# Kernel tuning notes

Hardware: AMD Instinct MI355X
Metric: run time of the kernel (lower is better)

The kernel has to match this reference:

```python
import jax, jax.numpy as jnp
import numpy as np

B, H, S, D = 4, 8, 2048, 64

def setup_inputs() -> dict:
    key = jax.random.key(0)
    k1, k2 = jax.random.split(key)
    q = jax.random.normal(k1, (B, H, S, D), dtype=jnp.float32)
    kv = jax.random.normal(k2, (B, H, S, D), dtype=jnp.float32)
    mask = jnp.zeros((1, 1, S, S), dtype=jnp.float32)
    return {"q": q, "kv": kv, "mask": mask}

def reference(q, kv, mask):
    # score = q @ kv^T / sqrt(d_k) + mask ; softmax over last dim ; @ kv
    d_k = jnp.asarray(kv.shape[-1], dtype=q.dtype)
    score = jnp.einsum('bhqd,bhkd->bhqk', q, kv) / jnp.sqrt(d_k)
    score = score + mask
    attn = jax.nn.softmax(score, axis=-1)
    out = jnp.einsum('bhqk,bhkd->bhqd', attn, kv)
    return out
```

## Files before the change

kernel.cpp:

```cpp
#include <hip/hip_runtime.h>
#include <hip/hip_bf16.h>
#include <stdint.h>


typedef __bf16 bf16;
typedef __attribute__((ext_vector_type(8))) __bf16 bf16x8;
typedef __attribute__((ext_vector_type(4))) __bf16 bf16x4;
typedef __attribute__((ext_vector_type(4))) float floatx4;
typedef __attribute__((ext_vector_type(16))) float floatx16;
typedef __attribute__((ext_vector_type(4))) int int4v;
typedef __attribute__((ext_vector_type(2))) unsigned int uint2v;

#define SLEN 2048
#define DH   64
#define BR   64
#define BC   64
#define NKT  (SLEN / BC)
#define NQT  (SLEN / BR)
#define BH_N 32
#define LOG2E 1.44269504088896341f

#define IMGE_G 4096

#define AS1 __attribute__((address_space(1)))
#define AS3 __attribute__((address_space(3)))

static __device__ inline float fexp2(float x) {
    return __builtin_amdgcn_exp2f(x);
}

static_assert(BH_N == NQT, "prep kernel folds bh and qt onto one grid axis");

__global__ __launch_bounds__(256) void kv_prep(
    const float* __restrict__ kv, const float* __restrict__ mask,
    bf16* __restrict__ kvK, bf16* __restrict__ kvT, int* __restrict__ flags)
{
    __shared__ bf16 Tl[64 * 72];
    __shared__ int wany[4];
    const int kt = blockIdx.x, z = blockIdx.y;
    const int t = threadIdx.x;

    float acc = 0.f;
#pragma unroll
    for (int i = 0; i < 4; ++i) {
        int f = i * 256 + t;
        int row = f >> 4, c4 = (f & 15) * 4;
        const float4 v = *(const float4*)(mask + (size_t)(z * BR + row) * SLEN + kt * BC + c4);
        acc = fmaxf(acc, fmaxf(fmaxf(fabsf(v.x), fabsf(v.y)), fmaxf(fabsf(v.z), fabsf(v.w))));
    }
    unsigned long long any = __ballot(acc != 0.f);
    if ((t & 63) == 0) wany[t >> 6] = (any != 0ull) ? 1 : 0;

    const float* src = kv + ((size_t)z * SLEN + kt * BC) * DH;
#pragma unroll
    for (int i = 0; i < 4; ++i) {
        int f = i * 256 + t;
        int key = f >> 4, d4 = (f & 15) * 4;
        float4 v = *(const float4*)(src + (size_t)key * DH + d4);
        bf16x4 b; b[0] = (bf16)v.x; b[1] = (bf16)v.y; b[2] = (bf16)v.z; b[3] = (bf16)v.w;
        *(bf16x4*)&Tl[key * 72 + d4] = b;
    }
    __syncthreads();
    if (t == 0) flags[z * NKT + kt] = wany[0] | wany[1] | wany[2] | wany[3];

    bf16* outK = kvK + ((size_t)z * NKT + kt) * IMGE_G;
#pragma unroll
    for (int i = 0; i < 2; ++i) {
        int G = i * 256 + t;
        int u = G >> 8, ss = (G >> 6) & 3, ln = G & 63;
        int key = u * 32 + (ln & 31), d0 = 16 * ss + 8 * (ln >> 5);
        bf16x8 w = *(const bf16x8*)&Tl[key * 72 + d0];
        *(bf16x8*)(outK + (size_t)G * 8) = w;
    }
    bf16* outV = kvT + ((size_t)z * NKT + kt) * IMGE_G;
#pragma unroll
    for (int i = 0; i < 2; ++i) {
        int G = i * 256 + t;
        int dt = G >> 8, u = (G >> 7) & 1, ff = (G >> 6) & 1, ln = G & 63;
        int d = dt * 32 + (ln & 31), kb = u * 32 + 16 * ff + 8 * (ln >> 5);
        bf16x8 w;
#pragma unroll
        for (int j = 0; j < 8; ++j)
            w[j] = Tl[(kb + j) * 72 + d];
        *(bf16x8*)(outV + (size_t)G * 8) = w;
    }
}

__global__ __launch_bounds__(512, 2) void attn_fwd19(
    const float* __restrict__ q, const float* __restrict__ mask,
    const int* __restrict__ flags,
    const bf16* __restrict__ kvK, const bf16* __restrict__ kvT,
    float* __restrict__ out)
{
    __shared__ __align__(16) float Obuf[4 * 2 * 4 * 64 * 4];
    __shared__ float Lbuf[4 * 64];

    const int bh = blockIdx.x;
    const int qt = blockIdx.y;
    const int q0 = qt * 128;
    const int t = threadIdx.x;
    const int w = t >> 6, lane = t & 63;
    const int qg = w & 3, kh = w >> 2;
    const int r5 = lane & 31, h = lane >> 5;

    const float qscale = 0.125f * LOG2E;
    bf16x8 qf[4];
    {
        const float* qrow = q + ((size_t)bh * SLEN + q0 + qg * 32 + r5) * DH;
#pragma unroll
        for (int s = 0; s < 4; ++s) {
            float4 f0 = *(const float4*)(qrow + 16 * s + 8 * h);
            float4 f1 = *(const float4*)(qrow + 16 * s + 8 * h + 4);
            bf16x8 a;
            a[0] = (bf16)(f0.x * qscale); a[1] = (bf16)(f0.y * qscale);
            a[2] = (bf16)(f0.z * qscale); a[3] = (bf16)(f0.w * qscale);
            a[4] = (bf16)(f1.x * qscale); a[5] = (bf16)(f1.y * qscale);
            a[6] = (bf16)(f1.z * qscale); a[7] = (bf16)(f1.w * qscale);
            qf[s] = a;
        }
    }

    const int fqt = qt * 2 + (qg >> 1);
    unsigned fmask;
    {
        int ld = (lane < 32) ? flags[fqt * NKT + lane] : 0;
        fmask = (unsigned)__ballot(ld != 0);
    }

    floatx16 o[2];
#pragma unroll
    for (int dt = 0; dt < 2; ++dt)
#pragma unroll
        for (int i = 0; i < 16; ++i) o[dt][i] = 0.f;
    float l_run = 0.f;

    const char* Kb = (const char*)(kvK + (size_t)bh * NKT * IMGE_G) + lane * 16;
    const char* Vb = (const char*)(kvT + (size_t)bh * NKT * IMGE_G) + lane * 16;

    for (int e = 0; e < 16; ++e) {
        const int kt = kh * 16 + e;
        const char* Kt = Kb + (size_t)kt * 8192;
        const char* Vt = Vb + (size_t)kt * 8192;
        const bool dm = (fmask >> kt) & 1u;

#pragma unroll
        for (int u = 0; u < 2; ++u) {
            floatx16 s;
#pragma unroll
            for (int i = 0; i < 16; ++i) s[i] = 0.f;
            {
                const char* Ku = Kt + u * 4096;
                bf16x8 kf0 = *(const bf16x8*)(Ku);
                bf16x8 kf1 = *(const bf16x8*)(Ku + 1024);
                bf16x8 kf2 = *(const bf16x8*)(Ku + 2048);
                bf16x8 kf3 = *(const bf16x8*)(Ku + 3072);
                s = __builtin_amdgcn_mfma_f32_32x32x16_bf16(kf0, qf[0], s, 0, 0, 0);
                s = __builtin_amdgcn_mfma_f32_32x32x16_bf16(kf1, qf[1], s, 0, 0, 0);
                s = __builtin_amdgcn_mfma_f32_32x32x16_bf16(kf2, qf[2], s, 0, 0, 0);
                s = __builtin_amdgcn_mfma_f32_32x32x16_bf16(kf3, qf[3], s, 0, 0, 0);
            }

            if (dm) {
                const float* mrow = mask + (size_t)(q0 + qg * 32 + r5) * SLEN
                                    + kt * 64 + u * 32 + 4 * h;
#pragma unroll
                for (int g4 = 0; g4 < 4; ++g4) {
                    float4 mv = *(const float4*)(mrow + 8 * g4);
                    s[4 * g4 + 0] += mv.x * LOG2E;
                    s[4 * g4 + 1] += mv.y * LOG2E;
                    s[4 * g4 + 2] += mv.z * LOG2E;
                    s[4 * g4 + 3] += mv.w * LOG2E;
                }
            }

            const char* Vu = Vt + u * 2048;
            bf16x8 v00 = *(const bf16x8*)(Vu);
            bf16x8 v01 = *(const bf16x8*)(Vu + 1024);
            bf16x8 v10 = *(const bf16x8*)(Vu + 4096);
            bf16x8 v11 = *(const bf16x8*)(Vu + 4096 + 1024);

#pragma unroll
            for (int i = 0; i < 16; ++i) s[i] = fexp2(s[i]);
            l_run += ((s[0] + s[1]) + (s[2] + s[3]))
                   + ((s[4] + s[5]) + (s[6] + s[7]))
                   + ((s[8] + s[9]) + (s[10] + s[11]))
                   + ((s[12] + s[13]) + (s[14] + s[15]));

            bf16x4 lA = { (bf16)s[0],  (bf16)s[1],  (bf16)s[2],  (bf16)s[3]  };
            bf16x4 hA = { (bf16)s[4],  (bf16)s[5],  (bf16)s[6],  (bf16)s[7]  };
            bf16x4 lB = { (bf16)s[8],  (bf16)s[9],  (bf16)s[10], (bf16)s[11] };
            bf16x4 hB = { (bf16)s[12], (bf16)s[13], (bf16)s[14], (bf16)s[15] };
            uint2v xA = __builtin_bit_cast(uint2v, lA);
            uint2v yA = __builtin_bit_cast(uint2v, hA);
            uint2v xB = __builtin_bit_cast(uint2v, lB);
            uint2v yB = __builtin_bit_cast(uint2v, hB);
            uint2v sA0 = __builtin_amdgcn_permlane32_swap(xA[0], yA[0], false, false);
            uint2v sA1 = __builtin_amdgcn_permlane32_swap(xA[1], yA[1], false, false);
            uint2v sB0 = __builtin_amdgcn_permlane32_swap(xB[0], yB[0], false, false);
            uint2v sB1 = __builtin_amdgcn_permlane32_swap(xB[1], yB[1], false, false);
            int4v pAi = { (int)sA0[0], (int)sA1[0], (int)sA0[1], (int)sA1[1] };
            int4v pBi = { (int)sB0[0], (int)sB1[0], (int)sB0[1], (int)sB1[1] };
            bf16x8 pfA = __builtin_bit_cast(bf16x8, pAi);
            bf16x8 pfB = __builtin_bit_cast(bf16x8, pBi);

            o[0] = __builtin_amdgcn_mfma_f32_32x32x16_bf16(v00, pfA, o[0], 0, 0, 0);
            o[0] = __builtin_amdgcn_mfma_f32_32x32x16_bf16(v01, pfB, o[0], 0, 0, 0);
            o[1] = __builtin_amdgcn_mfma_f32_32x32x16_bf16(v10, pfA, o[1], 0, 0, 0);
            o[1] = __builtin_amdgcn_mfma_f32_32x32x16_bf16(v11, pfB, o[1], 0, 0, 0);
        }
    }

    __syncthreads();
    if (kh == 1) {
#pragma unroll
        for (int dt = 0; dt < 2; ++dt)
#pragma unroll
            for (int k = 0; k < 4; ++k) {
                float4 v;
                v.x = o[dt][4 * k + 0]; v.y = o[dt][4 * k + 1];
                v.z = o[dt][4 * k + 2]; v.w = o[dt][4 * k + 3];
                *(float4*)(Obuf + ((size_t)((qg * 2 + dt) * 4 + k) * 64 + lane) * 4) = v;
            }
        Lbuf[qg * 64 + lane] = l_run;
    }
    __syncthreads();
    if (kh == 0) {
        float lsum = l_run + Lbuf[qg * 64 + lane];
        float l = lsum + __shfl_xor(lsum, 32);
        float inv = 1.f / l;
        float* ob = out + ((size_t)bh * SLEN + q0 + qg * 32 + r5) * DH + 4 * h;
#pragma unroll
        for (int dt = 0; dt < 2; ++dt)
#pragma unroll
            for (int k = 0; k < 4; ++k) {
                float4 p = *(const float4*)(Obuf + ((size_t)((qg * 2 + dt) * 4 + k) * 64 + lane) * 4);
                float4 v;
                v.x = (o[dt][4 * k + 0] + p.x) * inv;
                v.y = (o[dt][4 * k + 1] + p.y) * inv;
                v.z = (o[dt][4 * k + 2] + p.z) * inv;
                v.w = (o[dt][4 * k + 3] + p.w) * inv;
                *(float4*)(ob + dt * 32 + 8 * k) = v;
            }
    }
}

#define LDT 72
__global__ __launch_bounds__(256) void attn_mask_flags(
    const float* __restrict__ mask, int* __restrict__ flags)
{
    const int kt = blockIdx.x, qt = blockIdx.y;
    const int t = threadIdx.x;
    float acc = 0.f;
#pragma unroll
    for (int i = 0; i < 4; ++i) {
        int f = i * 256 + t;
        int row = f >> 4, c4 = (f & 15) * 4;
        const float4 v = *(const float4*)(mask + (size_t)(qt * BR + row) * SLEN + kt * BC + c4);
        acc = fmaxf(acc, fmaxf(fmaxf(fabsf(v.x), fabsf(v.y)), fmaxf(fabsf(v.z), fabsf(v.w))));
    }
    unsigned long long any = __ballot(acc != 0.f);
    __shared__ int wany[4];
    if ((t & 63) == 0) wany[t >> 6] = (any != 0ull) ? 1 : 0;
    __syncthreads();
    if (t == 0) flags[qt * NKT + kt] = wany[0] | wany[1] | wany[2] | wany[3];
}

__global__ __launch_bounds__(256) void attn_fwd(
    const float* __restrict__ q, const float* __restrict__ kv,
    const float* __restrict__ mask, const int* __restrict__ flags,
    float* __restrict__ out)
{
    __shared__ __align__(16) bf16 Kl[BC * LDT];
    __shared__ __align__(16) bf16 Vt[DH * LDT];
    __shared__ __align__(16) bf16 Pl[BR * LDT];

    const int qt = blockIdx.x;
    const int bh = blockIdx.y;
    const int q0 = qt * BR;
    const int t = threadIdx.x;
    const int wave = t >> 6, lane = t & 63;
    const int ln16 = lane & 15, quad = lane >> 4;

    const float qscale = 0.125f * LOG2E;
    bf16x8 aq[2];
    {
        const float* qrow = q + ((size_t)bh * SLEN + q0 + wave * 16 + ln16) * DH;
#pragma unroll
        for (int kc = 0; kc < 2; ++kc) {
            float4 f0 = *(const float4*)(qrow + kc * 32 + quad * 8);
            float4 f1 = *(const float4*)(qrow + kc * 32 + quad * 8 + 4);
            bf16x8 a;
            a[0] = (bf16)(f0.x * qscale); a[1] = (bf16)(f0.y * qscale);
            a[2] = (bf16)(f0.z * qscale); a[3] = (bf16)(f0.w * qscale);
            a[4] = (bf16)(f1.x * qscale); a[5] = (bf16)(f1.y * qscale);
            a[6] = (bf16)(f1.z * qscale); a[7] = (bf16)(f1.w * qscale);
            aq[kc] = a;
        }
    }

    floatx4 o[4];
#pragma unroll
    for (int dt = 0; dt < 4; ++dt) o[dt] = (floatx4){0.f, 0.f, 0.f, 0.f};
    float m_run[4], l_run[4];
#pragma unroll
    for (int r = 0; r < 4; ++r) { m_run[r] = -3.0e38f; l_run[r] = 0.f; }

    const float* kvb = kv + (size_t)bh * SLEN * DH;

    for (int kt = 0; kt < NKT; ++kt) {
        float4 st[4];
        const float* kvt = kvb + (size_t)kt * BC * DH;
#pragma unroll
        for (int i = 0; i < 4; ++i) {
            int f = i * 256 + t;
            st[i] = *(const float4*)(kvt + (size_t)f * 4);
        }
        __syncthreads();
#pragma unroll
        for (int i = 0; i < 4; ++i) {
            int f = i * 256 + t;
            int key = f >> 4, d4 = (f & 15) * 4;
            bf16 b0 = (bf16)st[i].x, b1 = (bf16)st[i].y, b2 = (bf16)st[i].z, b3 = (bf16)st[i].w;
            *(bf16x4*)&Kl[key * LDT + d4] = (bf16x4){b0, b1, b2, b3};
            Vt[(d4 + 0) * LDT + key] = b0;
            Vt[(d4 + 1) * LDT + key] = b1;
            Vt[(d4 + 2) * LDT + key] = b2;
            Vt[(d4 + 3) * LDT + key] = b3;
        }
        __syncthreads();

        floatx4 s[4];
#pragma unroll
        for (int nt = 0; nt < 4; ++nt) {
            s[nt] = (floatx4){0.f, 0.f, 0.f, 0.f};
#pragma unroll
            for (int kc = 0; kc < 2; ++kc) {
                bf16x8 bk = *(const bf16x8*)&Kl[(ln16 + 16 * nt) * LDT + kc * 32 + quad * 8];
                s[nt] = __builtin_amdgcn_mfma_f32_16x16x32_bf16(aq[kc], bk, s[nt], 0, 0, 0);
            }
        }

        if (!flags || flags[qt * NKT + kt]) {
            const float* mrow = mask + (size_t)(q0 + quad * 4) * SLEN + kt * BC + ln16;
#pragma unroll
            for (int r = 0; r < 4; ++r)
#pragma unroll
                for (int nt = 0; nt < 4; ++nt)
                    s[nt][r] += mrow[(size_t)r * SLEN + nt * 16] * LOG2E;
        }

#pragma unroll
        for (int r = 0; r < 4; ++r) {
            float mx = fmaxf(fmaxf(s[0][r], s[1][r]), fmaxf(s[2][r], s[3][r]));
            mx = fmaxf(mx, __shfl_xor(mx, 1));
            mx = fmaxf(mx, __shfl_xor(mx, 2));
            mx = fmaxf(mx, __shfl_xor(mx, 4));
            mx = fmaxf(mx, __shfl_xor(mx, 8));
            float mnew = fmaxf(m_run[r], mx);
            float alpha = exp2f(m_run[r] - mnew);
            m_run[r] = mnew;
            float rs = 0.f;
#pragma unroll
            for (int nt = 0; nt < 4; ++nt) {
                float p = exp2f(s[nt][r] - mnew);
                s[nt][r] = p;
                rs += p;
            }
            rs += __shfl_xor(rs, 1);
            rs += __shfl_xor(rs, 2);
            rs += __shfl_xor(rs, 4);
            rs += __shfl_xor(rs, 8);
            l_run[r] = l_run[r] * alpha + rs;
#pragma unroll
            for (int dt = 0; dt < 4; ++dt) o[dt][r] *= alpha;
        }

#pragma unroll
        for (int nt = 0; nt < 4; ++nt)
#pragma unroll
            for (int r = 0; r < 4; ++r)
                Pl[(wave * 16 + quad * 4 + r) * LDT + ln16 + 16 * nt] = (bf16)s[nt][r];

#pragma unroll
        for (int kc2 = 0; kc2 < 2; ++kc2) {
            bf16x8 pfr = *(const bf16x8*)&Pl[(wave * 16 + ln16) * LDT + kc2 * 32 + quad * 8];
#pragma unroll
            for (int dt = 0; dt < 4; ++dt) {
                bf16x8 vfr = *(const bf16x8*)&Vt[(ln16 + 16 * dt) * LDT + kc2 * 32 + quad * 8];
                o[dt] = __builtin_amdgcn_mfma_f32_16x16x32_bf16(pfr, vfr, o[dt], 0, 0, 0);
            }
        }
    }

#pragma unroll
    for (int r = 0; r < 4; ++r) {
        float inv = 1.0f / l_run[r];
        int qrow = q0 + wave * 16 + quad * 4 + r;
        float* orow = out + ((size_t)bh * SLEN + qrow) * DH;
#pragma unroll
        for (int dt = 0; dt < 4; ++dt)
            orow[ln16 + 16 * dt] = o[dt][r] * inv;
    }
}

extern "C" void kernel_launch(void* const* d_in, const int* in_sizes, int n_in,
                              void* d_out, int out_size, void* d_ws, size_t ws_size,
                              hipStream_t stream)
{
    const float* q    = (const float*)d_in[0];
    const float* kv   = (const float*)d_in[1];
    const float* mask = (const float*)d_in[2];
    float* out = (float*)d_out;

    const size_t kvKoff = 4096;
    const size_t kvToff = kvKoff + (size_t)BH_N * NKT * IMGE_G * 2;
    const size_t need   = kvToff + (size_t)BH_N * NKT * IMGE_G * 2;

    if (ws_size >= need) {
        int*  flags = (int*)d_ws;
        bf16* kvK   = (bf16*)((char*)d_ws + kvKoff);
        bf16* kvT   = (bf16*)((char*)d_ws + kvToff);
        kv_prep<<<dim3(NKT, BH_N), 256, 0, stream>>>(kv, mask, kvK, kvT, flags);
        attn_fwd19<<<dim3(BH_N, SLEN / 128), 512, 0, stream>>>(q, mask, flags, kvK, kvT, out);
    } else {
        int* flags = nullptr;
        if (ws_size >= (size_t)NQT * NKT * sizeof(int)) {
            flags = (int*)d_ws;
            attn_mask_flags<<<dim3(NKT, NQT), 256, 0, stream>>>(mask, flags);
        }
        attn_fwd<<<dim3(NQT, BH_N), 256, 0, stream>>>(q, kv, mask, flags, out);
    }
}
```

Baseline: 136.4 us.

## Shrink attention blocks to 64 query rows and double-buffer K/V register loads

The attention kernel now uses 256-thread blocks covering 64 query rows instead of 512 threads over 128 rows, doubling the grid size and halving shared memory per block. The key loop is restructured into a software pipeline: K and V fragments for the next sub-tile are loaded into a second register set while the current one is computed. The aim is to hide global-load latency and improve occupancy, at the cost of more registers for the double buffer and each block reusing K/V across fewer query rows.

```diff
diff --git a/kernel.cpp b/kernel.cpp
--- a/kernel.cpp
+++ b/kernel.cpp
@@ -86,21 +86,21 @@
     }
 }
 
-__global__ __launch_bounds__(512, 2) void attn_fwd19(
+__global__ __launch_bounds__(256) void attn_fwd20(
     const float* __restrict__ q, const float* __restrict__ mask,
     const int* __restrict__ flags,
     const bf16* __restrict__ kvK, const bf16* __restrict__ kvT,
     float* __restrict__ out)
 {
-    __shared__ __align__(16) float Obuf[4 * 2 * 4 * 64 * 4];
-    __shared__ float Lbuf[4 * 64];
+    __shared__ __align__(16) float Obuf[2 * 2 * 4 * 64 * 4];
+    __shared__ float Lbuf[2 * 64];
 
     const int bh = blockIdx.x;
     const int qt = blockIdx.y;
-    const int q0 = qt * 128;
+    const int q0 = qt * 64;
     const int t = threadIdx.x;
     const int w = t >> 6, lane = t & 63;
-    const int qg = w & 3, kh = w >> 2;
+    const int qg = w & 1, kh = w >> 1;
     const int r5 = lane & 31, h = lane >> 5;
 
     const float qscale = 0.125f * LOG2E;
@@ -120,10 +120,9 @@
         }
     }
 
-    const int fqt = qt * 2 + (qg >> 1);
     unsigned fmask;
     {
-        int ld = (lane < 32) ? flags[fqt * NKT + lane] : 0;
+        int ld = (lane < 32) ? flags[qt * NKT + lane] : 0;
         fmask = (unsigned)__ballot(ld != 0);
     }
 
@@ -137,78 +136,86 @@
     const char* Kb = (const char*)(kvK + (size_t)bh * NKT * IMGE_G) + lane * 16;
     const char* Vb = (const char*)(kvT + (size_t)bh * NKT * IMGE_G) + lane * 16;
 
-    for (int e = 0; e < 16; ++e) {
-        const int kt = kh * 16 + e;
-        const char* Kt = Kb + (size_t)kt * 8192;
-        const char* Vt = Vb + (size_t)kt * 8192;
-        const bool dm = (fmask >> kt) & 1u;
-
-#pragma unroll
-        for (int u = 0; u < 2; ++u) {
-            floatx16 s;
-#pragma unroll
-            for (int i = 0; i < 16; ++i) s[i] = 0.f;
-            {
-                const char* Ku = Kt + u * 4096;
-                bf16x8 kf0 = *(const bf16x8*)(Ku);
-                bf16x8 kf1 = *(const bf16x8*)(Ku + 1024);
-                bf16x8 kf2 = *(const bf16x8*)(Ku + 2048);
-                bf16x8 kf3 = *(const bf16x8*)(Ku + 3072);
-                s = __builtin_amdgcn_mfma_f32_32x32x16_bf16(kf0, qf[0], s, 0, 0, 0);
-                s = __builtin_amdgcn_mfma_f32_32x32x16_bf16(kf1, qf[1], s, 0, 0, 0);
-                s = __builtin_amdgcn_mfma_f32_32x32x16_bf16(kf2, qf[2], s, 0, 0, 0);
-                s = __builtin_amdgcn_mfma_f32_32x32x16_bf16(kf3, qf[3], s, 0, 0, 0);
-            }
-
-            if (dm) {
-                const float* mrow = mask + (size_t)(q0 + qg * 32 + r5) * SLEN
-                                    + kt * 64 + u * 32 + 4 * h;
-#pragma unroll
-                for (int g4 = 0; g4 < 4; ++g4) {
-                    float4 mv = *(const float4*)(mrow + 8 * g4);
-                    s[4 * g4 + 0] += mv.x * LOG2E;
-                    s[4 * g4 + 1] += mv.y * LOG2E;
-                    s[4 * g4 + 2] += mv.z * LOG2E;
-                    s[4 * g4 + 3] += mv.w * LOG2E;
-                }
-            }
-
-            const char* Vu = Vt + u * 2048;
-            bf16x8 v00 = *(const bf16x8*)(Vu);
-            bf16x8 v01 = *(const bf16x8*)(Vu + 1024);
-            bf16x8 v10 = *(const bf16x8*)(Vu + 4096);
-            bf16x8 v11 = *(const bf16x8*)(Vu + 4096 + 1024);
-
-#pragma unroll
-            for (int i = 0; i < 16; ++i) s[i] = fexp2(s[i]);
-            l_run += ((s[0] + s[1]) + (s[2] + s[3]))
-                   + ((s[4] + s[5]) + (s[6] + s[7]))
-                   + ((s[8] + s[9]) + (s[10] + s[11]))
-                   + ((s[12] + s[13]) + (s[14] + s[15]));
-
-            bf16x4 lA = { (bf16)s[0],  (bf16)s[1],  (bf16)s[2],  (bf16)s[3]  };
-            bf16x4 hA = { (bf16)s[4],  (bf16)s[5],  (bf16)s[6],  (bf16)s[7]  };
-            bf16x4 lB = { (bf16)s[8],  (bf16)s[9],  (bf16)s[10], (bf16)s[11] };
-            bf16x4 hB = { (bf16)s[12], (bf16)s[13], (bf16)s[14], (bf16)s[15] };
-            uint2v xA = __builtin_bit_cast(uint2v, lA);
-            uint2v yA = __builtin_bit_cast(uint2v, hA);
-            uint2v xB = __builtin_bit_cast(uint2v, lB);
-            uint2v yB = __builtin_bit_cast(uint2v, hB);
-            uint2v sA0 = __builtin_amdgcn_permlane32_swap(xA[0], yA[0], false, false);
-            uint2v sA1 = __builtin_amdgcn_permlane32_swap(xA[1], yA[1], false, false);
-            uint2v sB0 = __builtin_amdgcn_permlane32_swap(xB[0], yB[0], false, false);
-            uint2v sB1 = __builtin_amdgcn_permlane32_swap(xB[1], yB[1], false, false);
-            int4v pAi = { (int)sA0[0], (int)sA1[0], (int)sA0[1], (int)sA1[1] };
-            int4v pBi = { (int)sB0[0], (int)sB1[0], (int)sB0[1], (int)sB1[1] };
-            bf16x8 pfA = __builtin_bit_cast(bf16x8, pAi);
-            bf16x8 pfB = __builtin_bit_cast(bf16x8, pBi);
-
-            o[0] = __builtin_amdgcn_mfma_f32_32x32x16_bf16(v00, pfA, o[0], 0, 0, 0);
-            o[0] = __builtin_amdgcn_mfma_f32_32x32x16_bf16(v01, pfB, o[0], 0, 0, 0);
-            o[1] = __builtin_amdgcn_mfma_f32_32x32x16_bf16(v10, pfA, o[1], 0, 0, 0);
-            o[1] = __builtin_amdgcn_mfma_f32_32x32x16_bf16(v11, pfB, o[1], 0, 0, 0);
-        }
-    }
+    bf16x8 ka0, ka1, ka2, ka3, va0, va1, va2, va3;
+    bf16x8 kb0, kb1, kb2, kb3, vb0, vb1, vb2, vb3;
+
+#define LOAD_SUB(K0,K1,K2,K3,V0,V1,V2,V3, j)                                  \
+    {                                                                          \
+        const int jj = (j) & 31;                                               \
+        const char* Kt = Kb + (size_t)(kh * 16 + (jj >> 1)) * 8192 + (jj & 1) * 4096; \
+        const char* Vt = Vb + (size_t)(kh * 16 + (jj >> 1)) * 8192 + (jj & 1) * 2048; \
+        K0 = *(const bf16x8*)(Kt);                                             \
+        K1 = *(const bf16x8*)(Kt + 1024);                                      \
+        K2 = *(const bf16x8*)(Kt + 2048);                                      \
+        K3 = *(const bf16x8*)(Kt + 3072);                                      \
+        V0 = *(const bf16x8*)(Vt);                                             \
+        V1 = *(const bf16x8*)(Vt + 1024);                                      \
+        V2 = *(const bf16x8*)(Vt + 4096);                                      \
+        V3 = *(const bf16x8*)(Vt + 4096 + 1024);                               \
+    }
+
+#define COMPUTE_SUB(K0,K1,K2,K3,V0,V1,V2,V3, j)                               \
+    {                                                                          \
+        const int jj = (j);                                                    \
+        const int kt_ = kh * 16 + (jj >> 1);                                   \
+        floatx16 s;                                                            \
+        _Pragma("unroll")                                                      \
+        for (int i = 0; i < 16; ++i) s[i] = 0.f;                               \
+        s = __builtin_amdgcn_mfma_f32_32x32x16_bf16(K0, qf[0], s, 0, 0, 0);    \
+        s = __builtin_amdgcn_mfma_f32_32x32x16_bf16(K1, qf[1], s, 0, 0, 0);    \
+        s = __builtin_amdgcn_mfma_f32_32x32x16_bf16(K2, qf[2], s, 0, 0, 0);    \
+        s = __builtin_amdgcn_mfma_f32_32x32x16_bf16(K3, qf[3], s, 0, 0, 0);    \
+        if ((fmask >> kt_) & 1u) {                                             \
+            const float* mrow = mask + (size_t)(q0 + qg * 32 + r5) * SLEN      \
+                                + kt_ * 64 + (jj & 1) * 32 + 4 * h;            \
+            _Pragma("unroll")                                                  \
+            for (int g4 = 0; g4 < 4; ++g4) {                                   \
+                float4 mv = *(const float4*)(mrow + 8 * g4);                   \
+                s[4 * g4 + 0] += mv.x * LOG2E;                                 \
+                s[4 * g4 + 1] += mv.y * LOG2E;                                 \
+                s[4 * g4 + 2] += mv.z * LOG2E;                                 \
+                s[4 * g4 + 3] += mv.w * LOG2E;                                 \
+            }                                                                  \
+        }                                                                      \
+        _Pragma("unroll")                                                      \
+        for (int i = 0; i < 16; ++i) s[i] = fexp2(s[i]);                       \
+        l_run += ((s[0] + s[1]) + (s[2] + s[3]))                               \
+               + ((s[4] + s[5]) + (s[6] + s[7]))                               \
+               + ((s[8] + s[9]) + (s[10] + s[11]))                             \
+               + ((s[12] + s[13]) + (s[14] + s[15]));                          \
+        bf16x4 lA = { (bf16)s[0],  (bf16)s[1],  (bf16)s[2],  (bf16)s[3]  };    \
+        bf16x4 hA = { (bf16)s[4],  (bf16)s[5],  (bf16)s[6],  (bf16)s[7]  };    \
+        bf16x4 lB = { (bf16)s[8],  (bf16)s[9],  (bf16)s[10], (bf16)s[11] };    \
+        bf16x4 hB = { (bf16)s[12], (bf16)s[13], (bf16)s[14], (bf16)s[15] };    \
+        uint2v xA = __builtin_bit_cast(uint2v, lA);                            \
+        uint2v yA = __builtin_bit_cast(uint2v, hA);                            \
+        uint2v xB = __builtin_bit_cast(uint2v, lB);                            \
+        uint2v yB = __builtin_bit_cast(uint2v, hB);                            \
+        uint2v sA0 = __builtin_amdgcn_permlane32_swap(xA[0], yA[0], false, false); \
+        uint2v sA1 = __builtin_amdgcn_permlane32_swap(xA[1], yA[1], false, false); \
+        uint2v sB0 = __builtin_amdgcn_permlane32_swap(xB[0], yB[0], false, false); \
+        uint2v sB1 = __builtin_amdgcn_permlane32_swap(xB[1], yB[1], false, false); \
+        int4v pAi = { (int)sA0[0], (int)sA1[0], (int)sA0[1], (int)sA1[1] };    \
+        int4v pBi = { (int)sB0[0], (int)sB1[0], (int)sB0[1], (int)sB1[1] };    \
+        bf16x8 pfA = __builtin_bit_cast(bf16x8, pAi);                          \
+        bf16x8 pfB = __builtin_bit_cast(bf16x8, pBi);                          \
+        o[0] = __builtin_amdgcn_mfma_f32_32x32x16_bf16(V0, pfA, o[0], 0, 0, 0); \
+        o[0] = __builtin_amdgcn_mfma_f32_32x32x16_bf16(V1, pfB, o[0], 0, 0, 0); \
+        o[1] = __builtin_amdgcn_mfma_f32_32x32x16_bf16(V2, pfA, o[1], 0, 0, 0); \
+        o[1] = __builtin_amdgcn_mfma_f32_32x32x16_bf16(V3, pfB, o[1], 0, 0, 0); \
+    }
+
+    LOAD_SUB(ka0, ka1, ka2, ka3, va0, va1, va2, va3, 0)
+
+    for (int it = 0; it < 16; ++it) {
+        const int j0 = 2 * it, j1 = 2 * it + 1;
+        LOAD_SUB(kb0, kb1, kb2, kb3, vb0, vb1, vb2, vb3, j1)
+        COMPUTE_SUB(ka0, ka1, ka2, ka3, va0, va1, va2, va3, j0)
+        LOAD_SUB(ka0, ka1, ka2, ka3, va0, va1, va2, va3, j1 + 1)
+        COMPUTE_SUB(kb0, kb1, kb2, kb3, vb0, vb1, vb2, vb3, j1)
+    }
+#undef LOAD_SUB
+#undef COMPUTE_SUB
 
     __syncthreads();
     if (kh == 1) {
@@ -421,7 +428,7 @@
         bf16* kvK   = (bf16*)((char*)d_ws + kvKoff);
         bf16* kvT   = (bf16*)((char*)d_ws + kvToff);
         kv_prep<<<dim3(NKT, BH_N), 256, 0, stream>>>(kv, mask, kvK, kvT, flags);
-        attn_fwd19<<<dim3(BH_N, SLEN / 128), 512, 0, stream>>>(q, mask, flags, kvK, kvT, out);
+        attn_fwd20<<<dim3(BH_N, SLEN / 64), 256, 0, stream>>>(q, mask, flags, kvK, kvT, out);
     } else {
         int* flags = nullptr;
         if (ws_size >= (size_t)NQT * NKT * sizeof(int)) {
```

Measured after the change: 139.4 us. 1.02x slower.
